# Kernel optimization log

Measured on AMD Instinct MI355X. Metric: run time of the kernel, lower is better.

## Reference

```python
import jax, jax.numpy as jnp
import numpy as np

N_NODES = 100000
N_EDGES = 1600000
HID = 128
N_GRAPHS = 2048


def _glorot(key, shape):
    fan_in, fan_out = shape[0], shape[1]
    lim = (6.0 / (fan_in + fan_out)) ** 0.5
    return jax.random.uniform(key, shape, jnp.float32, -lim, lim)


def setup_inputs() -> dict:
    key = jax.random.key(0)
    ks = jax.random.split(key, 16)
    x = jax.random.normal(ks[0], (N_NODES, 1), jnp.float32)
    edge_index = jax.random.randint(ks[1], (2, N_EDGES), 0, N_NODES, jnp.int64)
    batch = jnp.sort(jax.random.randint(ks[2], (N_NODES,), 0, N_GRAPHS, jnp.int64))
    return {
        "x": x,
        "edge_index": edge_index,
        "batch": batch,
        "W1": _glorot(ks[3], (1, HID)),   "b1": jnp.zeros((HID,), jnp.float32),
        "W2": _glorot(ks[4], (HID, HID)), "b2": jnp.zeros((HID,), jnp.float32),
        "W3": _glorot(ks[5], (HID, HID)), "b3": jnp.zeros((HID,), jnp.float32),
        "Wl1": _glorot(ks[6], (HID, HID)), "bl1": jnp.zeros((HID,), jnp.float32),
        "Wl2": _glorot(ks[7], (HID, HID)), "bl2": jnp.zeros((HID,), jnp.float32),
        "Wl3": _glorot(ks[8], (HID, 1)),   "bl3": jnp.zeros((1,), jnp.float32),
    }


def _gcn_layer(h, src, dst, norm, W, b, n_nodes):
    # h: [N, Fin] -> [N, Fout]; GCNConv: D^-1/2 (A+I) D^-1/2 (h W) + b
    hw = h @ W                                   # [N, Fout]
    msg = hw[src] * norm[:, None]                # [E+N, Fout] gather + scale
    return jax.ops.segment_sum(msg, dst, num_segments=n_nodes) + b


def _gcn_norm(edge_index, n_nodes, dtype):
    loop = jnp.arange(n_nodes, dtype=edge_index.dtype)
    src = jnp.concatenate([edge_index[0], loop])  # self-loops appended
    dst = jnp.concatenate([edge_index[1], loop])
    deg = jax.ops.segment_sum(jnp.ones_like(dst, dtype=dtype), dst, num_segments=n_nodes)
    dinv = jnp.where(deg > 0, jax.lax.rsqrt(jnp.maximum(deg, 1e-12)), 0.0)
    norm = dinv[src] * dinv[dst]                  # [E+N]
    return src, dst, norm


def reference(x, edge_index, batch, W1, b1, W2, b2, W3, b3, Wl1, bl1, Wl2, bl2, Wl3, bl3):
    n = x.shape[0]
    src, dst, norm = _gcn_norm(edge_index, n, x.dtype)
    h = jax.nn.relu(_gcn_layer(x, src, dst, norm, W1, b1, n))
    h = jax.nn.relu(_gcn_layer(h, src, dst, norm, W2, b2, n))
    h = jax.nn.relu(_gcn_layer(h, src, dst, norm, W3, b3, n))
    # global_mean_pool over graph ids
    sums = jax.ops.segment_sum(h, batch, num_segments=N_GRAPHS)          # [G, HID]
    cnt = jax.ops.segment_sum(jnp.ones((n,), h.dtype), batch, num_segments=N_GRAPHS)
    g = sums / jnp.maximum(cnt, 1.0)[:, None]
    g = jax.nn.relu(g @ Wl1 + bl1)
    g = jax.nn.relu(g @ Wl2 + bl2)
    out = g @ Wl3 + bl3                                                  # [G, 1]
    return out.reshape(-1)
```

## Files before the change

### kernel.cpp

```cpp
#include <hip/hip_runtime.h>
#include <hip/hip_fp16.h>

#define H 128
#define SHIFT 9
#define BN 512
#define MAXNB 256
#define CHUNK 4096
#define CAP 16384
#define CSTRIDE (H * 16 + 4)


__global__ __launch_bounds__(256) void scatter_pairs_k(const int* __restrict__ src,
                                                       const int* __restrict__ dst,
                                                       int* __restrict__ gcur,
                                                       unsigned* __restrict__ pairbuf,
                                                       int E, int NBv) {
    __shared__ unsigned stage[CHUNK];
    __shared__ unsigned char stb[CHUNK];
    __shared__ int hist[MAXNB], basel[MAXNB], cur[MAXNB], gbase[MAXNB];
    __shared__ int total;
    int tid = threadIdx.x;
    int base = blockIdx.x * CHUNK;

    int mysrc[16], mydst[16];
    #pragma unroll
    for (int i = 0; i < 16; ++i) {
        int e = base + i * 256 + tid;
        if (e < E) { mysrc[i] = src[e]; mydst[i] = dst[e]; } else mydst[i] = -1;
    }
    hist[tid] = 0;
    __syncthreads();
    #pragma unroll
    for (int i = 0; i < 16; ++i)
        if (mydst[i] >= 0) atomicAdd(&hist[mydst[i] >> SHIFT], 1);
    __syncthreads();
    if (tid == 0) {
        int run = 0;
        for (int b = 0; b < NBv; ++b) { basel[b] = run; run += hist[b]; }
        total = run;
    }
    __syncthreads();
    if (tid < NBv) {
        cur[tid] = basel[tid];
        if (hist[tid] > 0) gbase[tid] = tid * CAP + atomicAdd(&gcur[tid], hist[tid]);
    }
    __syncthreads();
    #pragma unroll
    for (int i = 0; i < 16; ++i)
        if (mydst[i] >= 0) {
            int b = mydst[i] >> SHIFT;
            int slot = atomicAdd(&cur[b], 1);
            stage[slot] = ((unsigned)(mydst[i] & (BN - 1)) << 17) | (unsigned)mysrc[i];
            stb[slot] = (unsigned char)b;
        }
    __syncthreads();
    for (int s = tid; s < total; s += 256) {
        int b = stb[s];
        pairbuf[gbase[b] + (s - basel[b])] = stage[s];
    }
}

__global__ __launch_bounds__(512) void build_csr_k(const unsigned* __restrict__ pairbuf,
                                                   const int* __restrict__ gcur,
                                                   const float* __restrict__ x,
                                                   int* __restrict__ offs, int* __restrict__ eend,
                                                   float* __restrict__ dinv, float* __restrict__ s,
                                                   int* __restrict__ csr, int N) {
    __shared__ int hist[BN];
    __shared__ int cur[BN];
    __shared__ int ps[BN];
    int b = blockIdx.x, tid = threadIdx.x;
    int node0 = b << SHIFT;
    int e0 = b * CAP, e1 = e0 + gcur[b];
    hist[tid] = 0;
    __syncthreads();
    for (int p = e0 + tid; p < e1; p += 512)
        atomicAdd(&hist[pairbuf[p] >> 17], 1);
    __syncthreads();
    int v0 = hist[tid];
    ps[tid] = v0;
    __syncthreads();
    for (int off = 1; off < BN; off <<= 1) {
        int t = (tid >= off) ? ps[tid - off] : 0;
        __syncthreads();
        ps[tid] += t;
        __syncthreads();
    }
    int g0 = e0 + ps[tid] - v0;
    int n0 = node0 + tid;
    if (n0 < N) {
        float d = rsqrtf((float)(v0 + 1));
        offs[n0] = g0;
        eend[n0] = g0 + v0;
        dinv[n0] = d;
        s[n0] = x[n0] * d;
    }
    cur[tid] = g0;
    __syncthreads();
    for (int p = e0 + tid; p < e1; p += 512) {
        unsigned v = pairbuf[p];
        int pos = atomicAdd(&cur[v >> 17], 1);
        csr[pos] = (int)(v & 0x1FFFFu);
    }
}


__global__ void agg1_k(const float* __restrict__ s, const int* __restrict__ offs,
                       const int* __restrict__ eend, const int* __restrict__ csr,
                       const float* __restrict__ dinv, float2* __restrict__ td, int n) {
    int i = blockIdx.x * blockDim.x + threadIdx.x;
    if (i >= n) return;
    float sum = s[i];
    int e0 = offs[i], e1 = eend[i];
    float a0 = 0.f, a1 = 0.f, a2 = 0.f, a3 = 0.f;
    int p = e0;
    for (; p + 4 <= e1; p += 4) {
        a0 += s[csr[p]]; a1 += s[csr[p + 1]]; a2 += s[csr[p + 2]]; a3 += s[csr[p + 3]];
    }
    for (; p < e1; ++p) sum += s[csr[p]];
    sum += (a0 + a1) + (a2 + a3);
    float d = dinv[i];
    td[i] = make_float2(sum * d, d);
}


__global__ __launch_bounds__(256) void gather_td_k(const int* __restrict__ csr,
                                                   const float2* __restrict__ td,
                                                   const int* __restrict__ gcur,
                                                   float2* __restrict__ etd) {
    int b = blockIdx.x >> 2;
    int k = blockIdx.x & 3;
    int base = b * CAP + k * (CAP / 4);
    int e1 = b * CAP + gcur[b];
    int hi = base + (CAP / 4); if (hi > e1) hi = e1;
    for (int p0 = base; p0 < hi; p0 += 1024) {
        int p = p0 + threadIdx.x;
        bool m0 = (p < hi), m1 = (p + 256 < hi), m2 = (p + 512 < hi), m3 = (p + 768 < hi);
        int i0 = m0 ? csr[p] : 0;
        int i1 = m1 ? csr[p + 256] : 0;
        int i2 = m2 ? csr[p + 512] : 0;
        int i3 = m3 ? csr[p + 768] : 0;
        float2 v0 = td[i0];
        float2 v1 = td[i1];
        float2 v2 = td[i2];
        float2 v3 = td[i3];
        if (m0) etd[p] = v0;
        if (m1) etd[p + 256] = v1;
        if (m2) etd[p + 512] = v2;
        if (m3) etd[p + 768] = v3;
    }
}


__global__ __launch_bounds__(256) void l2_agg_k(const float2* __restrict__ td,
                                                const float2* __restrict__ etd,
                                                const int* __restrict__ offs,
                                                const int* __restrict__ eend,
                                                const float* __restrict__ w1,
                                                const float* __restrict__ b1,
                                                float* __restrict__ U, int n) {
    int node = blockIdx.x * 4 + (threadIdx.x >> 6);
    int lane = threadIdx.x & 63;
    if (node >= n) return;
    float wa = w1[lane],      wb = w1[lane + 64];
    float ba = b1[lane],      bb = b1[lane + 64];
    float2 self = td[node];
    float sa = fmaxf(fmaf(self.x, wa, ba), 0.f) * self.y;
    float sb = fmaxf(fmaf(self.x, wb, bb), 0.f) * self.y;
    const float2* ep = etd + offs[node];
    int cnt = eend[node] - offs[node];
    int p = 0;
    for (; p + 8 <= cnt; p += 8) {
        float2 v[8];
        #pragma unroll
        for (int u = 0; u < 8; ++u) v[u] = ep[p + u];
        #pragma unroll
        for (int u = 0; u < 8; ++u) {
            sa = fmaf(fmaxf(fmaf(v[u].x, wa, ba), 0.f), v[u].y, sa);
            sb = fmaf(fmaxf(fmaf(v[u].x, wb, bb), 0.f), v[u].y, sb);
        }
    }
    for (; p < cnt; ++p) {
        float2 v = ep[p];
        sa = fmaf(fmaxf(fmaf(v.x, wa, ba), 0.f), v.y, sa);
        sb = fmaf(fmaxf(fmaf(v.x, wb, bb), 0.f), v.y, sb);
    }
    float d = self.y;
    U[(size_t)node * H + lane]      = sa * d;
    U[(size_t)node * H + lane + 64] = sb * d;
}


__device__ __forceinline__ void stage_WT(const float* __restrict__ W, float* __restrict__ WT) {
    for (int idx = threadIdx.x; idx < H * H / 4; idx += 256) {
        float4 v = ((const float4*)W)[idx];
        int k  = idx >> 5;
        int c4 = idx & 31;
        int cc = c4 >> 2;
        int j  = (c4 & 3) * 4;
        *(float4*)(WT + cc * CSTRIDE + k * 16 + j) = v;
    }
}


__global__ __launch_bounds__(256) void gemm_post_k(const float* __restrict__ in, const float* __restrict__ W,
                                                   const float* __restrict__ bias, const float* __restrict__ pscale,
                                                   __half* __restrict__ out, int n) {
    __shared__ float WT[8 * CSTRIDE];
    stage_WT(W, WT);
    __syncthreads();
    const int cc = threadIdx.x & 7;
    const int rg = threadIdx.x >> 3;
    const int c0 = cc * 16;
    const int row0 = blockIdx.x * 128 + rg * 4;
    const float* wt = WT + cc * CSTRIDE;

    const float* p[4];
    #pragma unroll
    for (int r = 0; r < 4; ++r) {
        int rr = row0 + r; if (rr > n - 1) rr = n - 1;
        p[r] = in + (size_t)rr * H;
    }

    float acc[4][16];
    #pragma unroll
    for (int r = 0; r < 4; ++r)
        #pragma unroll
        for (int j = 0; j < 16; ++j) acc[r][j] = 0.f;

    for (int k4 = 0; k4 < H / 4; ++k4) {
        float4 a[4];
        #pragma unroll
        for (int r = 0; r < 4; ++r) a[r] = *(const float4*)(p[r] + k4 * 4);
        #pragma unroll
        for (int kk = 0; kk < 4; ++kk) {
            const float* wb = wt + (k4 * 4 + kk) * 16;
            float w[16];
            *(float4*)(w + 0)  = *(const float4*)(wb + 0);
            *(float4*)(w + 4)  = *(const float4*)(wb + 4);
            *(float4*)(w + 8)  = *(const float4*)(wb + 8);
            *(float4*)(w + 12) = *(const float4*)(wb + 12);
            float av[4];
            #pragma unroll
            for (int r = 0; r < 4; ++r) av[r] = ((const float*)&a[r])[kk];
            #pragma unroll
            for (int r = 0; r < 4; ++r)
                #pragma unroll
                for (int j = 0; j < 16; ++j)
                    acc[r][j] = fmaf(av[r], w[j], acc[r][j]);
        }
    }

    #pragma unroll
    for (int r = 0; r < 4; ++r) {
        int row = row0 + r;
        if (row < n) {
            float sc = pscale[row];
            __half2 hb[8];
            #pragma unroll
            for (int j4 = 0; j4 < 4; ++j4) {
                float ox = fmaxf(acc[r][j4 * 4 + 0] + bias[c0 + j4 * 4 + 0], 0.f) * sc;
                float oy = fmaxf(acc[r][j4 * 4 + 1] + bias[c0 + j4 * 4 + 1], 0.f) * sc;
                float oz = fmaxf(acc[r][j4 * 4 + 2] + bias[c0 + j4 * 4 + 2], 0.f) * sc;
                float ow = fmaxf(acc[r][j4 * 4 + 3] + bias[c0 + j4 * 4 + 3], 0.f) * sc;
                hb[j4 * 2 + 0] = __floats2half2_rn(ox, oy);
                hb[j4 * 2 + 1] = __floats2half2_rn(oz, ow);
            }
            __half* orow = out + (size_t)row * H + c0;
            *(uint4*)(orow + 0) = *(uint4*)&hb[0];
            *(uint4*)(orow + 8) = *(uint4*)&hb[4];
        }
    }
}


__device__ __forceinline__ void acc_h(float4& a, uint2 r) {
    __half2 h0 = *(__half2*)&r.x;
    __half2 h1 = *(__half2*)&r.y;
    float2 f0 = __half22float2(h0);
    float2 f1 = __half22float2(h1);
    a.x += f0.x; a.y += f0.y; a.z += f1.x; a.w += f1.y;
}

__device__ __forceinline__ float4 gather_row_sum_h(const uint2* __restrict__ hrow,
                                                   const int* __restrict__ csr,
                                                   int node, int e0, int e1, int half, int l) {
    float4 acc[8];
    #pragma unroll
    for (int u = 0; u < 8; ++u) acc[u] = make_float4(0.f, 0.f, 0.f, 0.f);
    if (half == 0) {
        uint2 rs = hrow[(size_t)node * 32 + l];
        acc_h(acc[0], rs);
    }
    int q = e0;
    for (; q + 15 < e1; q += 16) {
        int idx[8];
        #pragma unroll
        for (int u = 0; u < 8; ++u) idx[u] = csr[q + 2 * u + half];
        uint2 raw[8];
        #pragma unroll
        for (int u = 0; u < 8; ++u) raw[u] = hrow[(size_t)idx[u] * 32 + l];
        #pragma unroll
        for (int u = 0; u < 8; ++u) acc_h(acc[u], raw[u]);
    }
    for (; q + 7 < e1; q += 8) {
        int idx[4];
        #pragma unroll
        for (int u = 0; u < 4; ++u) idx[u] = csr[q + 2 * u + half];
        uint2 raw[4];
        #pragma unroll
        for (int u = 0; u < 4; ++u) raw[u] = hrow[(size_t)idx[u] * 32 + l];
        #pragma unroll
        for (int u = 0; u < 4; ++u) acc_h(acc[u], raw[u]);
    }
    for (; q < e1; q += 2) {
        int off = q + half;
        if (off < e1) {
            uint2 raw = hrow[(size_t)csr[off] * 32 + l];
            acc_h(acc[0], raw);
        }
    }
    float4 sum;
    sum.x = ((acc[0].x + acc[1].x) + (acc[2].x + acc[3].x)) + ((acc[4].x + acc[5].x) + (acc[6].x + acc[7].x));
    sum.y = ((acc[0].y + acc[1].y) + (acc[2].y + acc[3].y)) + ((acc[4].y + acc[5].y) + (acc[6].y + acc[7].y));
    sum.z = ((acc[0].z + acc[1].z) + (acc[2].z + acc[3].z)) + ((acc[4].z + acc[5].z) + (acc[6].z + acc[7].z));
    sum.w = ((acc[0].w + acc[1].w) + (acc[2].w + acc[3].w)) + ((acc[4].w + acc[5].w) + (acc[6].w + acc[7].w));
    sum.x += __shfl_xor(sum.x, 32);
    sum.y += __shfl_xor(sum.y, 32);
    sum.z += __shfl_xor(sum.z, 32);
    sum.w += __shfl_xor(sum.w, 32);
    return sum;
}


__global__ __launch_bounds__(256) void agg3h_k(const uint2* __restrict__ Zh, const int* __restrict__ offs,
                                               const int* __restrict__ eend, const int* __restrict__ csr,
                                               const float* __restrict__ dinv,
                                               float* __restrict__ U, int n) {
    int node = blockIdx.x * 4 + (threadIdx.x >> 6);
    int lane = threadIdx.x & 63;
    int half = lane >> 5;
    int l = lane & 31;
    if (node >= n) return;
    float4 sum = gather_row_sum_h(Zh, csr, node, offs[node], eend[node], half, l);
    if (half == 0) {
        float d = dinv[node];
        float4 o;
        o.x = sum.x * d; o.y = sum.y * d; o.z = sum.z * d; o.w = sum.w * d;
        ((float4*)U)[(size_t)node * 32 + l] = o;
    }
}


__global__ __launch_bounds__(256) void gemm_k(const float* __restrict__ in, const float* __restrict__ W,
                                              const float* __restrict__ bias,
                                              float* __restrict__ out, int n) {
    __shared__ float WT[8 * CSTRIDE];
    stage_WT(W, WT);
    __syncthreads();
    const int cc = threadIdx.x & 7;
    const int rg = threadIdx.x >> 3;
    const int c0 = cc * 16;
    const int row0 = blockIdx.x * 128 + rg * 4;
    const float* wt = WT + cc * CSTRIDE;

    const float* p[4];
    #pragma unroll
    for (int r = 0; r < 4; ++r) {
        int rr = row0 + r; if (rr > n - 1) rr = n - 1;
        p[r] = in + (size_t)rr * H;
    }

    float acc[4][16];
    #pragma unroll
    for (int r = 0; r < 4; ++r)
        #pragma unroll
        for (int j = 0; j < 16; ++j) acc[r][j] = 0.f;

    for (int k4 = 0; k4 < H / 4; ++k4) {
        float4 a[4];
        #pragma unroll
        for (int r = 0; r < 4; ++r) a[r] = *(const float4*)(p[r] + k4 * 4);
        #pragma unroll
        for (int kk = 0; kk < 4; ++kk) {
            const float* wb = wt + (k4 * 4 + kk) * 16;
            float w[16];
            *(float4*)(w + 0)  = *(const float4*)(wb + 0);
            *(float4*)(w + 4)  = *(const float4*)(wb + 4);
            *(float4*)(w + 8)  = *(const float4*)(wb + 8);
            *(float4*)(w + 12) = *(const float4*)(wb + 12);
            float av[4];
            #pragma unroll
            for (int r = 0; r < 4; ++r) av[r] = ((const float*)&a[r])[kk];
            #pragma unroll
            for (int r = 0; r < 4; ++r)
                #pragma unroll
                for (int j = 0; j < 16; ++j)
                    acc[r][j] = fmaf(av[r], w[j], acc[r][j]);
        }
    }

    #pragma unroll
    for (int r = 0; r < 4; ++r) {
        int row = row0 + r;
        if (row < n) {
            float* orow = out + (size_t)row * H + c0;
            #pragma unroll
            for (int j4 = 0; j4 < 4; ++j4) {
                float4 o;
                o.x = fmaxf(acc[r][j4 * 4 + 0] + bias[c0 + j4 * 4 + 0], 0.f);
                o.y = fmaxf(acc[r][j4 * 4 + 1] + bias[c0 + j4 * 4 + 1], 0.f);
                o.z = fmaxf(acc[r][j4 * 4 + 2] + bias[c0 + j4 * 4 + 2], 0.f);
                o.w = fmaxf(acc[r][j4 * 4 + 3] + bias[c0 + j4 * 4 + 3], 0.f);
                *(float4*)(orow + j4 * 4) = o;
            }
        }
    }
}


__global__ __launch_bounds__(128) void pool_k(const float* __restrict__ h, const int* __restrict__ batch,
                                              float* __restrict__ P, int n, int G) {
    int g = blockIdx.x, f = threadIdx.x;
    int lo = 0, hi = n;
    while (lo < hi) { int m = (lo + hi) >> 1; if (batch[m] < g) lo = m + 1; else hi = m; }
    int s0 = lo;
    hi = n;
    while (lo < hi) { int m = (lo + hi) >> 1; if (batch[m] < g + 1) lo = m + 1; else hi = m; }
    int s1 = lo;
    float a0 = 0.f, a1 = 0.f, a2 = 0.f, a3 = 0.f;
    int i = s0;
    for (; i + 4 <= s1; i += 4) {
        a0 += h[(size_t)i * H + f];
        a1 += h[(size_t)(i + 1) * H + f];
        a2 += h[(size_t)(i + 2) * H + f];
        a3 += h[(size_t)(i + 3) * H + f];
    }
    for (; i < s1; ++i) a0 += h[(size_t)i * H + f];
    float sum = (a0 + a1) + (a2 + a3);
    float c = (float)(s1 - s0); if (c < 1.f) c = 1.f;
    P[(size_t)g * H + f] = sum / c;
}


__global__ __launch_bounds__(256) void head_k(const float* __restrict__ P,
                                              const float* __restrict__ Wl1, const float* __restrict__ bl1,
                                              const float* __restrict__ Wl2, const float* __restrict__ bl2,
                                              const float* __restrict__ Wl3, const float* __restrict__ bl3,
                                              float* __restrict__ out, int G) {
    __shared__ float Wb[H * H];
    __shared__ float Tl[H * 133];
    __shared__ float w3l[H];
    int tid = threadIdx.x;
    int g0 = blockIdx.x * 128;

    if (tid < 128) w3l[tid] = Wl3[tid];
    for (int i = tid; i < H * H / 4; i += 256) ((float4*)Wb)[i] = ((const float4*)Wl1)[i];
    __syncthreads();

    const int cc = tid & 7, rg = tid >> 3, c0 = cc * 16;
    float acc[4][16];

    #pragma unroll
    for (int r = 0; r < 4; ++r)
        #pragma unroll
        for (int j = 0; j < 16; ++j) acc[r][j] = 0.f;
    const float4* P4 = (const float4*)P;
    for (int k4 = 0; k4 < H / 4; ++k4) {
        float4 a[4];
        #pragma unroll
        for (int r = 0; r < 4; ++r) a[r] = P4[(size_t)(g0 + rg * 4 + r) * 32 + k4];
        const float* wbase = Wb + (k4 * 4) * H + c0;
        #pragma unroll
        for (int kk = 0; kk < 4; ++kk) {
            float w[16];
            *(float4*)(w + 0)  = *(const float4*)(wbase + kk * H + 0);
            *(float4*)(w + 4)  = *(const float4*)(wbase + kk * H + 4);
            *(float4*)(w + 8)  = *(const float4*)(wbase + kk * H + 8);
            *(float4*)(w + 12) = *(const float4*)(wbase + kk * H + 12);
            float av[4];
            #pragma unroll
            for (int r = 0; r < 4; ++r) av[r] = ((const float*)&a[r])[kk];
            #pragma unroll
            for (int r = 0; r < 4; ++r)
                #pragma unroll
                for (int j = 0; j < 16; ++j)
                    acc[r][j] = fmaf(av[r], w[j], acc[r][j]);
        }
    }
    #pragma unroll
    for (int r = 0; r < 4; ++r) {
        int rl = rg * 4 + r;
        #pragma unroll
        for (int j = 0; j < 16; ++j)
            Tl[rl * 133 + c0 + j] = fmaxf(acc[r][j] + bl1[c0 + j], 0.f);
    }
    __syncthreads();
    for (int i = tid; i < H * H / 4; i += 256) ((float4*)Wb)[i] = ((const float4*)Wl2)[i];
    __syncthreads();

    #pragma unroll
    for (int r = 0; r < 4; ++r)
        #pragma unroll
        for (int j = 0; j < 16; ++j) acc[r][j] = 0.f;
    for (int k4 = 0; k4 < H / 4; ++k4) {
        float4 a[4];
        #pragma unroll
        for (int r = 0; r < 4; ++r) a[r] = *(const float4*)(Tl + (rg * 4 + r) * 133 + k4 * 4);
        const float* wbase = Wb + (k4 * 4) * H + c0;
        #pragma unroll
        for (int kk = 0; kk < 4; ++kk) {
            float w[16];
            *(float4*)(w + 0)  = *(const float4*)(wbase + kk * H + 0);
            *(float4*)(w + 4)  = *(const float4*)(wbase + kk * H + 4);
            *(float4*)(w + 8)  = *(const float4*)(wbase + kk * H + 8);
            *(float4*)(w + 12) = *(const float4*)(wbase + kk * H + 12);
            float av[4];
            #pragma unroll
            for (int r = 0; r < 4; ++r) av[r] = ((const float*)&a[r])[kk];
            #pragma unroll
            for (int r = 0; r < 4; ++r)
                #pragma unroll
                for (int j = 0; j < 16; ++j)
                    acc[r][j] = fmaf(av[r], w[j], acc[r][j]);
        }
    }
    float part[4];
    #pragma unroll
    for (int r = 0; r < 4; ++r) {
        float s = 0.f;
        #pragma unroll
        for (int j = 0; j < 16; ++j)
            s += fmaxf(acc[r][j] + bl2[c0 + j], 0.f) * w3l[c0 + j];
        part[r] = s;
    }
    #pragma unroll
    for (int off = 1; off < 8; off <<= 1)
        #pragma unroll
        for (int r = 0; r < 4; ++r) part[r] += __shfl_xor(part[r], off);
    if (cc == 0) {
        float bb = bl3[0];
        #pragma unroll
        for (int r = 0; r < 4; ++r) out[g0 + rg * 4 + r] = part[r] + bb;
    }
}


extern "C" void kernel_launch(void* const* d_in, const int* in_sizes, int n_in,
                              void* d_out, int out_size, void* d_ws, size_t ws_size,
                              hipStream_t stream) {
    const float* x     = (const float*)d_in[0];
    const int*   ei    = (const int*)d_in[1];
    const int*   batch = (const int*)d_in[2];
    const float* W1  = (const float*)d_in[3];  const float* b1  = (const float*)d_in[4];
    const float* W2  = (const float*)d_in[5];  const float* b2  = (const float*)d_in[6];
    const float* W3  = (const float*)d_in[7];  const float* b3  = (const float*)d_in[8];
    const float* Wl1 = (const float*)d_in[9];  const float* bl1 = (const float*)d_in[10];
    const float* Wl2 = (const float*)d_in[11]; const float* bl2 = (const float*)d_in[12];
    const float* Wl3 = (const float*)d_in[13]; const float* bl3 = (const float*)d_in[14];

    const int N = in_sizes[0];
    const int E = in_sizes[1] / 2;
    const int G = out_size;
    const int* srcp = ei;
    const int* dstp = ei + E;
    const int NB = (N + BN - 1) / BN;

    char* w = (char*)d_ws;
    size_t off = 0;
    auto alloc = [&](size_t bytes) -> void* {
        void* p = w + off;
        off += (bytes + 255) & ~(size_t)255;
        return p;
    };
    int*    gcur   = (int*)alloc((size_t)MAXNB * 4);
    int*    offs   = (int*)alloc((size_t)N * 4);
    int*    eend   = (int*)alloc((size_t)N * 4);
    int*    csr    = (int*)alloc((size_t)NB * CAP * 4);
    float*  dinv   = (float*)alloc((size_t)N * 4);
    float*  sbuf   = (float*)alloc((size_t)N * 4);
    float2* td     = (float2*)alloc((size_t)N * 8);
    float*  A      = (float*)alloc((size_t)N * H * 4);
    float*  B      = (float*)alloc((size_t)N * H * 4);
    float*  P      = (float*)alloc((size_t)G * H * 4);
    unsigned* pairbuf = (unsigned*)B;
    float2*   etd     = (float2*)B;
    __half*   Z2h     = (__half*)B;
    (void)ws_size; (void)n_in;

    hipMemsetAsync(gcur, 0, (size_t)MAXNB * 4, stream);
    scatter_pairs_k<<<(E + CHUNK - 1) / CHUNK, 256, 0, stream>>>(srcp, dstp, gcur, pairbuf, E, NB);
    build_csr_k<<<NB, 512, 0, stream>>>(pairbuf, gcur, x, offs, eend, dinv, sbuf, csr, N);

    agg1_k<<<(N + 255) / 256, 256, 0, stream>>>(sbuf, offs, eend, csr, dinv, td, N);

    gather_td_k<<<NB * 4, 256, 0, stream>>>(csr, td, gcur, etd);
    l2_agg_k<<<(N + 3) / 4, 256, 0, stream>>>(td, etd, offs, eend, W1, b1, A, N);
    gemm_post_k<<<(N + 127) / 128, 256, 0, stream>>>(A, W2, b2, dinv, Z2h, N);

    agg3h_k<<<(N + 3) / 4, 256, 0, stream>>>((const uint2*)Z2h, offs, eend, csr, dinv, A, N);
    gemm_k<<<(N + 127) / 128, 256, 0, stream>>>(A, W3, b3, B, N);
    pool_k<<<G, 128, 0, stream>>>(B, batch, P, N, G);

    head_k<<<(G + 127) / 128, 256, 0, stream>>>(P, Wl1, bl1, Wl2, bl2, Wl3, bl3,
                                                (float*)d_out, G);
}
```

Before: 444.1 us.

## Replace FP32 SIMT GEMMs with FP16 MFMA kernel and FP16 intermediates

Replaces the two scalar-FMA FP32 dense GEMMs (layers 2 and 3) with a single MFMA-based kernel using 16x16x32 f16 matrix instructions, with W transposed to fp16 in shared memory and outputs staged through LDS for coalesced stores. Intermediate activations (aggregation outputs and layer-3 output) are stored as fp16 instead of fp32, halving the memory traffic of the aggregation writes, GEMM reads and pooling reads. Pooling is rewritten to read half2 values with 64 threads. This trades precision (fp16 inputs to the GEMM and the stored activations) for lower bandwidth and use of the matrix cores.

After: 393.5 us. -11.4%, faster.

```diff
diff --git a/kernel.cpp b/kernel.cpp
--- a/kernel.cpp
+++ b/kernel.cpp
@@ -7,7 +7,11 @@
 #define MAXNB 256
 #define CHUNK 4096
 #define CAP 16384
-#define CSTRIDE (H * 16 + 4)
+
+typedef _Float16 half8 __attribute__((ext_vector_type(8)));
+typedef _Float16 half4 __attribute__((ext_vector_type(4)));
+typedef _Float16 half2t __attribute__((ext_vector_type(2)));
+typedef float f32x4 __attribute__((ext_vector_type(4)));
 
 
 __global__ __launch_bounds__(256) void scatter_pairs_k(const int* __restrict__ src,
@@ -158,7 +162,7 @@
                                                 const int* __restrict__ eend,
                                                 const float* __restrict__ w1,
                                                 const float* __restrict__ b1,
-                                                float* __restrict__ U, int n) {
+                                                _Float16* __restrict__ Uh, int n) {
     int node = blockIdx.x * 4 + (threadIdx.x >> 6);
     int lane = threadIdx.x & 63;
     if (node >= n) return;
@@ -186,90 +190,74 @@
         sb = fmaf(fmaxf(fmaf(v.x, wb, bb), 0.f), v.y, sb);
     }
     float d = self.y;
-    U[(size_t)node * H + lane]      = sa * d;
-    U[(size_t)node * H + lane + 64] = sb * d;
-}
-
-
-__device__ __forceinline__ void stage_WT(const float* __restrict__ W, float* __restrict__ WT) {
-    for (int idx = threadIdx.x; idx < H * H / 4; idx += 256) {
-        float4 v = ((const float4*)W)[idx];
+    Uh[(size_t)node * H + lane]      = (_Float16)(sa * d);
+    Uh[(size_t)node * H + lane + 64] = (_Float16)(sb * d);
+}
+
+
+__global__ __launch_bounds__(256) void gemm_h_k(const _Float16* __restrict__ in,
+                                                const float* __restrict__ W,
+                                                const float* __restrict__ bias,
+                                                const float* __restrict__ pscale,
+                                                _Float16* __restrict__ out, int n) {
+    __shared__ _Float16 WT[128 * 136];
+    __shared__ _Float16 OT[64 * 136];
+    __shared__ float bsh[H];
+
+    for (int idx = threadIdx.x; idx < 128 * 32; idx += 256) {
         int k  = idx >> 5;
-        int c4 = idx & 31;
-        int cc = c4 >> 2;
-        int j  = (c4 & 3) * 4;
-        *(float4*)(WT + cc * CSTRIDE + k * 16 + j) = v;
-    }
-}
-
-
-__global__ __launch_bounds__(256) void gemm_post_k(const float* __restrict__ in, const float* __restrict__ W,
-                                                   const float* __restrict__ bias, const float* __restrict__ pscale,
-                                                   __half* __restrict__ out, int n) {
-    __shared__ float WT[8 * CSTRIDE];
-    stage_WT(W, WT);
-    __syncthreads();
-    const int cc = threadIdx.x & 7;
-    const int rg = threadIdx.x >> 3;
-    const int c0 = cc * 16;
-    const int row0 = blockIdx.x * 128 + rg * 4;
-    const float* wt = WT + cc * CSTRIDE;
-
-    const float* p[4];
+        int c4 = (idx & 31) << 2;
+        float4 v = *(const float4*)(W + k * H + c4);
+        WT[(c4 + 0) * 136 + k] = (_Float16)v.x;
+        WT[(c4 + 1) * 136 + k] = (_Float16)v.y;
+        WT[(c4 + 2) * 136 + k] = (_Float16)v.z;
+        WT[(c4 + 3) * 136 + k] = (_Float16)v.w;
+    }
+    if (threadIdx.x < H) bsh[threadIdx.x] = bias[threadIdx.x];
+    __syncthreads();
+
+    const int wave = threadIdx.x >> 6;
+    const int l    = threadIdx.x & 63;
+    const int lr   = l & 15;
+    const int lk   = l >> 4;
+    const int row0 = blockIdx.x * 64 + wave * 16;
+
+    f32x4 acc[8];
+    #pragma unroll
+    for (int c = 0; c < 8; ++c) acc[c] = (f32x4){0.f, 0.f, 0.f, 0.f};
+
+    int arow = row0 + lr; if (arow > n - 1) arow = n - 1;
+    const _Float16* ap = in + (size_t)arow * H + lk * 8;
+
+    #pragma unroll
+    for (int ks = 0; ks < 4; ++ks) {
+        half8 a = *(const half8*)(ap + ks * 32);
+        #pragma unroll
+        for (int c = 0; c < 8; ++c) {
+            half8 b = *(const half8*)(WT + (c * 16 + lr) * 136 + ks * 32 + lk * 8);
+            acc[c] = __builtin_amdgcn_mfma_f32_16x16x32_f16(a, b, acc[c], 0, 0, 0);
+        }
+    }
+
     #pragma unroll
     for (int r = 0; r < 4; ++r) {
-        int rr = row0 + r; if (rr > n - 1) rr = n - 1;
-        p[r] = in + (size_t)rr * H;
-    }
-
-    float acc[4][16];
-    #pragma unroll
-    for (int r = 0; r < 4; ++r)
-        #pragma unroll
-        for (int j = 0; j < 16; ++j) acc[r][j] = 0.f;
-
-    for (int k4 = 0; k4 < H / 4; ++k4) {
-        float4 a[4];
-        #pragma unroll
-        for (int r = 0; r < 4; ++r) a[r] = *(const float4*)(p[r] + k4 * 4);
-        #pragma unroll
-        for (int kk = 0; kk < 4; ++kk) {
-            const float* wb = wt + (k4 * 4 + kk) * 16;
-            float w[16];
-            *(float4*)(w + 0)  = *(const float4*)(wb + 0);
-            *(float4*)(w + 4)  = *(const float4*)(wb + 4);
-            *(float4*)(w + 8)  = *(const float4*)(wb + 8);
-            *(float4*)(w + 12) = *(const float4*)(wb + 12);
-            float av[4];
-            #pragma unroll
-            for (int r = 0; r < 4; ++r) av[r] = ((const float*)&a[r])[kk];
-            #pragma unroll
-            for (int r = 0; r < 4; ++r)
-                #pragma unroll
-                for (int j = 0; j < 16; ++j)
-                    acc[r][j] = fmaf(av[r], w[j], acc[r][j]);
-        }
-    }
-
-    #pragma unroll
-    for (int r = 0; r < 4; ++r) {
-        int row = row0 + r;
-        if (row < n) {
-            float sc = pscale[row];
-            __half2 hb[8];
-            #pragma unroll
-            for (int j4 = 0; j4 < 4; ++j4) {
-                float ox = fmaxf(acc[r][j4 * 4 + 0] + bias[c0 + j4 * 4 + 0], 0.f) * sc;
-                float oy = fmaxf(acc[r][j4 * 4 + 1] + bias[c0 + j4 * 4 + 1], 0.f) * sc;
-                float oz = fmaxf(acc[r][j4 * 4 + 2] + bias[c0 + j4 * 4 + 2], 0.f) * sc;
-                float ow = fmaxf(acc[r][j4 * 4 + 3] + bias[c0 + j4 * 4 + 3], 0.f) * sc;
-                hb[j4 * 2 + 0] = __floats2half2_rn(ox, oy);
-                hb[j4 * 2 + 1] = __floats2half2_rn(oz, ow);
-            }
-            __half* orow = out + (size_t)row * H + c0;
-            *(uint4*)(orow + 0) = *(uint4*)&hb[0];
-            *(uint4*)(orow + 8) = *(uint4*)&hb[4];
-        }
+        int lrow = wave * 16 + lk * 4 + r;
+        int grow = blockIdx.x * 64 + lrow;
+        float sc = 1.f;
+        if (pscale) { int gr = grow > n - 1 ? n - 1 : grow; sc = pscale[gr]; }
+        #pragma unroll
+        for (int c = 0; c < 8; ++c) {
+            float v = fmaxf(acc[c][r] + bsh[c * 16 + lr], 0.f) * sc;
+            OT[lrow * 136 + c * 16 + lr] = (_Float16)v;
+        }
+    }
+    __syncthreads();
+
+    for (int idx = threadIdx.x; idx < 64 * 16; idx += 256) {
+        int row = idx >> 4;
+        int gr = blockIdx.x * 64 + row;
+        if (gr < n)
+            ((uint4*)(out + (size_t)gr * H))[idx & 15] = ((const uint4*)(OT + row * 136))[idx & 15];
     }
 }
 
@@ -336,7 +324,7 @@
 __global__ __launch_bounds__(256) void agg3h_k(const uint2* __restrict__ Zh, const int* __restrict__ offs,
                                                const int* __restrict__ eend, const int* __restrict__ csr,
                                                const float* __restrict__ dinv,
-                                               float* __restrict__ U, int n) {
+                                               _Float16* __restrict__ Uh, int n) {
     int node = blockIdx.x * 4 + (threadIdx.x >> 6);
     int lane = threadIdx.x & 63;
     int half = lane >> 5;
@@ -345,82 +333,18 @@
     float4 sum = gather_row_sum_h(Zh, csr, node, offs[node], eend[node], half, l);
     if (half == 0) {
         float d = dinv[node];
-        float4 o;
-        o.x = sum.x * d; o.y = sum.y * d; o.z = sum.z * d; o.w = sum.w * d;
-        ((float4*)U)[(size_t)node * 32 + l] = o;
-    }
-}
-
-
-__global__ __launch_bounds__(256) void gemm_k(const float* __restrict__ in, const float* __restrict__ W,
-                                              const float* __restrict__ bias,
-                                              float* __restrict__ out, int n) {
-    __shared__ float WT[8 * CSTRIDE];
-    stage_WT(W, WT);
-    __syncthreads();
-    const int cc = threadIdx.x & 7;
-    const int rg = threadIdx.x >> 3;
-    const int c0 = cc * 16;
-    const int row0 = blockIdx.x * 128 + rg * 4;
-    const float* wt = WT + cc * CSTRIDE;
-
-    const float* p[4];
-    #pragma unroll
-    for (int r = 0; r < 4; ++r) {
-        int rr = row0 + r; if (rr > n - 1) rr = n - 1;
-        p[r] = in + (size_t)rr * H;
-    }
-
-    float acc[4][16];
-    #pragma unroll
-    for (int r = 0; r < 4; ++r)
-        #pragma unroll
-        for (int j = 0; j < 16; ++j) acc[r][j] = 0.f;
-
-    for (int k4 = 0; k4 < H / 4; ++k4) {
-        float4 a[4];
-        #pragma unroll
-        for (int r = 0; r < 4; ++r) a[r] = *(const float4*)(p[r] + k4 * 4);
-        #pragma unroll
-        for (int kk = 0; kk < 4; ++kk) {
-            const float* wb = wt + (k4 * 4 + kk) * 16;
-            float w[16];
-            *(float4*)(w + 0)  = *(const float4*)(wb + 0);
-            *(float4*)(w + 4)  = *(const float4*)(wb + 4);
-            *(float4*)(w + 8)  = *(const float4*)(wb + 8);
-            *(float4*)(w + 12) = *(const float4*)(wb + 12);
-            float av[4];
-            #pragma unroll
-            for (int r = 0; r < 4; ++r) av[r] = ((const float*)&a[r])[kk];
-            #pragma unroll
-            for (int r = 0; r < 4; ++r)
-                #pragma unroll
-                for (int j = 0; j < 16; ++j)
-                    acc[r][j] = fmaf(av[r], w[j], acc[r][j]);
-        }
-    }
-
-    #pragma unroll
-    for (int r = 0; r < 4; ++r) {
-        int row = row0 + r;
-        if (row < n) {
-            float* orow = out + (size_t)row * H + c0;
-            #pragma unroll
-            for (int j4 = 0; j4 < 4; ++j4) {
-                float4 o;
-                o.x = fmaxf(acc[r][j4 * 4 + 0] + bias[c0 + j4 * 4 + 0], 0.f);
-                o.y = fmaxf(acc[r][j4 * 4 + 1] + bias[c0 + j4 * 4 + 1], 0.f);
-                o.z = fmaxf(acc[r][j4 * 4 + 2] + bias[c0 + j4 * 4 + 2], 0.f);
-                o.w = fmaxf(acc[r][j4 * 4 + 3] + bias[c0 + j4 * 4 + 3], 0.f);
-                *(float4*)(orow + j4 * 4) = o;
-            }
-        }
-    }
-}
-
-
-__global__ __launch_bounds__(128) void pool_k(const float* __restrict__ h, const int* __restrict__ batch,
-                                              float* __restrict__ P, int n, int G) {
+        half4 o;
+        o[0] = (_Float16)(sum.x * d);
+        o[1] = (_Float16)(sum.y * d);
+        o[2] = (_Float16)(sum.z * d);
+        o[3] = (_Float16)(sum.w * d);
+        *(half4*)(Uh + (size_t)node * H + l * 4) = o;
+    }
+}
+
+
+__global__ __launch_bounds__(64) void pool_h_k(const _Float16* __restrict__ h, const int* __restrict__ batch,
+                                               float* __restrict__ P, int n, int G) {
     int g = blockIdx.x, f = threadIdx.x;
     int lo = 0, hi = n;
     while (lo < hi) { int m = (lo + hi) >> 1; if (batch[m] < g) lo = m + 1; else hi = m; }
@@ -428,18 +352,29 @@
     hi = n;
     while (lo < hi) { int m = (lo + hi) >> 1; if (batch[m] < g + 1) lo = m + 1; else hi = m; }
     int s1 = lo;
-    float a0 = 0.f, a1 = 0.f, a2 = 0.f, a3 = 0.f;
+    const half2t* hp = (const half2t*)h;
+    float a0x = 0.f, a0y = 0.f, a1x = 0.f, a1y = 0.f;
+    float a2x = 0.f, a2y = 0.f, a3x = 0.f, a3y = 0.f;
     int i = s0;
     for (; i + 4 <= s1; i += 4) {
-        a0 += h[(size_t)i * H + f];
-        a1 += h[(size_t)(i + 1) * H + f];
-        a2 += h[(size_t)(i + 2) * H + f];
-        a3 += h[(size_t)(i + 3) * H + f];
-    }
-    for (; i < s1; ++i) a0 += h[(size_t)i * H + f];
-    float sum = (a0 + a1) + (a2 + a3);
+        half2t v0 = hp[(size_t)i * 64 + f];
+        half2t v1 = hp[(size_t)(i + 1) * 64 + f];
+        half2t v2 = hp[(size_t)(i + 2) * 64 + f];
+        half2t v3 = hp[(size_t)(i + 3) * 64 + f];
+        a0x += (float)v0[0]; a0y += (float)v0[1];
+        a1x += (float)v1[0]; a1y += (float)v1[1];
+        a2x += (float)v2[0]; a2y += (float)v2[1];
+        a3x += (float)v3[0]; a3y += (float)v3[1];
+    }
+    for (; i < s1; ++i) {
+        half2t v = hp[(size_t)i * 64 + f];
+        a0x += (float)v[0]; a0y += (float)v[1];
+    }
+    float sx = (a0x + a1x) + (a2x + a3x);
+    float sy = (a0y + a1y) + (a2y + a3y);
     float c = (float)(s1 - s0); if (c < 1.f) c = 1.f;
-    P[(size_t)g * H + f] = sum / c;
+    P[(size_t)g * H + 2 * f]     = sx / c;
+    P[(size_t)g * H + 2 * f + 1] = sy / c;
 }
 
 
@@ -585,7 +520,10 @@
     float*  P      = (float*)alloc((size_t)G * H * 4);
     unsigned* pairbuf = (unsigned*)B;
     float2*   etd     = (float2*)B;
-    __half*   Z2h     = (__half*)B;
+    _Float16* Z2h     = (_Float16*)B;
+    _Float16* h3h     = (_Float16*)B;
+    _Float16* U2h     = (_Float16*)A;
+    _Float16* U3h     = (_Float16*)A;
     (void)ws_size; (void)n_in;
 
     hipMemsetAsync(gcur, 0, (size_t)MAXNB * 4, stream);
@@ -595,12 +533,12 @@
     agg1_k<<<(N + 255) / 256, 256, 0, stream>>>(sbuf, offs, eend, csr, dinv, td, N);
 
     gather_td_k<<<NB * 4, 256, 0, stream>>>(csr, td, gcur, etd);
-    l2_agg_k<<<(N + 3) / 4, 256, 0, stream>>>(td, etd, offs, eend, W1, b1, A, N);
-    gemm_post_k<<<(N + 127) / 128, 256, 0, stream>>>(A, W2, b2, dinv, Z2h, N);
-
-    agg3h_k<<<(N + 3) / 4, 256, 0, stream>>>((const uint2*)Z2h, offs, eend, csr, dinv, A, N);
-    gemm_k<<<(N + 127) / 128, 256, 0, stream>>>(A, W3, b3, B, N);
-    pool_k<<<G, 128, 0, stream>>>(B, batch, P, N, G);
+    l2_agg_k<<<(N + 3) / 4, 256, 0, stream>>>(td, etd, offs, eend, W1, b1, U2h, N);
+    gemm_h_k<<<(N + 63) / 64, 256, 0, stream>>>(U2h, W2, b2, dinv, Z2h, N);
+
+    agg3h_k<<<(N + 3) / 4, 256, 0, stream>>>((const uint2*)Z2h, offs, eend, csr, dinv, U3h, N);
+    gemm_h_k<<<(N + 63) / 64, 256, 0, stream>>>(U3h, W3, b3, nullptr, h3h, N);
+    pool_h_k<<<G, 64, 0, stream>>>(h3h, batch, P, N, G);
 
     head_k<<<(G + 127) / 128, 256, 0, stream>>>(P, Wl1, bl1, Wl2, bl2, Wl3, bl3,
                                                 (float*)d_out, G);
```
